# Kernel tuning notes

Hardware: AMD Instinct MI355X
Metric: run time of the kernel (lower is better)

Reference implementation:

```python
import jax, jax.numpy as jnp
import numpy as np

B, S, V, E, HID = 16, 40, 1004, 256, 256
C, R, HW = 1024, 256, 32  # featureChannel, releMapChannel, spatial
BN_EPS = 1e-5


def setup_inputs() -> dict:
    key = jax.random.key(0)
    ks = jax.random.split(key, 16)
    sc = 0.05
    emb = jax.random.normal(ks[4], (V, E), jnp.float32) * sc
    emb = emb.at[0].set(0.0)  # padding_idx = 0
    return {
        "feature": jax.random.normal(ks[0], (B, C, HW, HW), jnp.float32),
        "depth": jax.random.uniform(ks[1], (B, 1, HW, HW), jnp.float32),
        "instruction_idx": jax.random.randint(ks[2], (B, S), 0, V, jnp.int32),
        "instruction_length": jnp.clip(jax.random.randint(ks[3], (B,), 1, S + 1, jnp.int32), 1, S),
        "only_train_rele": 1,
        "emb_table": emb,
        "w_ih": jax.random.normal(ks[5], (4 * HID, E), jnp.float32) * sc,
        "w_hh": jax.random.normal(ks[6], (4 * HID, HID), jnp.float32) * sc,
        "b_ih": jax.random.normal(ks[7], (4 * HID,), jnp.float32) * sc,
        "b_hh": jax.random.normal(ks[8], (4 * HID,), jnp.float32) * sc,
        "e2d_w": jax.random.normal(ks[9], (HID, HID), jnp.float32) * sc,
        "e2d_b": jax.random.normal(ks[10], (HID,), jnp.float32) * sc,
        "lin1_w": jax.random.normal(ks[11], (R * C, HID), jnp.float32) * sc,
        "lin1_b": jax.random.normal(ks[12], (R * C,), jnp.float32) * sc,
        "bn_gamma": jnp.ones((R,), jnp.float32),
        "bn_beta": jnp.zeros((R,), jnp.float32),
        "bn_mean": jax.random.normal(ks[13], (R,), jnp.float32) * 0.01,
        "bn_var": jnp.ones((R,), jnp.float32),
    }


def _encoder_lstm(idx, lengths, emb_table, w_ih, w_hh, b_ih, b_hh, e2d_w, e2d_b):
    # Faithful to packed-sequence LSTM: state stops updating at each sample's length.
    embeds = emb_table[idx]                      # [B,S,E]
    xs = jnp.swapaxes(embeds, 0, 1)              # [S,B,E]
    mask = (jnp.arange(S)[:, None] < lengths[None, :])  # [S,B]
    h0 = jnp.zeros((B, HID), embeds.dtype)
    c0 = jnp.zeros((B, HID), embeds.dtype)

    def step(carry, xm):
        h, c = carry
        x_t, m = xm                              # [B,E], [B]
        gates = x_t @ w_ih.T + h @ w_hh.T + (b_ih + b_hh)  # [B,4H]
        i, f, g, o = jnp.split(gates, 4, axis=-1)  # torch gate order: i,f,g,o
        c_new = jax.nn.sigmoid(f) * c + jax.nn.sigmoid(i) * jnp.tanh(g)
        h_new = jax.nn.sigmoid(o) * jnp.tanh(c_new)
        m = m[:, None]
        return (jnp.where(m, h_new, h), jnp.where(m, c_new, c)), None

    (h_t, _), _ = jax.lax.scan(step, (h0, c0), (xs, mask))
    return jnp.tanh(h_t @ e2d_w.T + e2d_b)       # [B,HID]


def reference(feature, depth, instruction_idx, instruction_length, only_train_rele,
              emb_table, w_ih, w_hh, b_ih, b_hh, e2d_w, e2d_b,
              lin1_w, lin1_b, bn_gamma, bn_beta, bn_mean, bn_var):
    instr = _encoder_lstm(instruction_idx, instruction_length, emb_table,
                          w_ih, w_hh, b_ih, b_hh, e2d_w, e2d_b)  # [B,HID]
    # per-sample dynamic 1x1 filters (dropout in eval mode -> identity)
    f1 = jax.nn.leaky_relu(instr @ lin1_w.T + lin1_b, negative_slope=0.01)
    f1 = f1.reshape(B, R, C)
    # batched per-sample 1x1 conv: one einsum replaces the batch loop of F.conv2d
    rele = jax.nn.relu(jnp.einsum('bchw,brc->brhw', feature, f1))  # [B,R,H,W]
    # BatchNorm2d in eval mode with running stats
    scale = bn_gamma / jnp.sqrt(bn_var + BN_EPS)
    rele = rele * scale[None, :, None, None] + (bn_beta - bn_mean * scale)[None, :, None, None]
    single = jnp.max(rele, axis=1)               # channel-max pooling -> [B,H,W]
    return jnp.clip(single, 0.0, 1.0)
```

## Files before the change

kernel.cpp:

```cpp
#include <hip/hip_runtime.h>
#include <hip/hip_fp16.h>
#include <math.h>

#define NB 16
#define SQ 40
#define HIDN 256
#define CC 1024
#define NROW 262144

#define AGENT __HIP_MEMORY_SCOPE_AGENT

__device__ __forceinline__ float sigf(float x){ return 1.0f/(1.0f+__expf(-x)); }

typedef _Float16 h2v __attribute__((ext_vector_type(2)));
typedef _Float16 f16x8 __attribute__((ext_vector_type(8)));
typedef float    f32x4 __attribute__((ext_vector_type(4)));

__device__ __forceinline__ float fd2(unsigned w, unsigned h, float acc){
  h2v a = __builtin_bit_cast(h2v, w);
  h2v b = __builtin_bit_cast(h2v, h);
#if __has_builtin(__builtin_amdgcn_fdot2)
  return __builtin_amdgcn_fdot2(a, b, acc, false);
#else
  return acc + (float)a.x*(float)b.x + (float)a.y*(float)b.y;
#endif
}

__device__ __forceinline__ unsigned pkh(float lo, float hi){
  return (unsigned)__half_as_ushort(__float2half_rn(lo))
       | ((unsigned)__half_as_ushort(__float2half_rn(hi)) << 16);
}

__global__ __launch_bounds__(256) void k_xgates(
    const int* __restrict__ idx, const float* __restrict__ emb,
    const float* __restrict__ w_ih, const float* __restrict__ b_ih,
    const float* __restrict__ b_hh, float* __restrict__ XG)
{
  __shared__ float xs[8*256];
  int t = threadIdx.x;
  int tb0 = blockIdx.x * 8;
  #pragma unroll
  for (int i = 0; i < 8; ++i) {
    int flat = t + i*256;
    int p = flat >> 8, k = flat & 255;
    int tb = tb0 + p;
    int ts = tb >> 4, b = tb & 15;
    int row = idx[b*SQ + ts];
    xs[p*256 + k] = emb[row*256 + k];
  }
  __syncthreads();
  int rows[4];
  float acc[4][8];
  #pragma unroll
  for (int r = 0; r < 4; ++r) {
    rows[r] = t + r*256;
    float bias = b_ih[rows[r]] + b_hh[rows[r]];
    #pragma unroll
    for (int p = 0; p < 8; ++p) acc[r][p] = bias;
  }
  for (int k16 = 0; k16 < 16; ++k16) {
    float4 w[4][4];
    #pragma unroll
    for (int r = 0; r < 4; ++r)
      #pragma unroll
      for (int q = 0; q < 4; ++q)
        w[r][q] = *(const float4*)&w_ih[rows[r]*256 + k16*16 + q*4];
    #pragma unroll
    for (int p = 0; p < 8; ++p) {
      #pragma unroll
      for (int q = 0; q < 4; ++q) {
        float4 x = *(const float4*)&xs[p*256 + k16*16 + q*4];
        #pragma unroll
        for (int r = 0; r < 4; ++r)
          acc[r][p] += w[r][q].x*x.x + w[r][q].y*x.y + w[r][q].z*x.z + w[r][q].w*x.w;
      }
    }
  }
  #pragma unroll
  for (int p = 0; p < 8; ++p)
    #pragma unroll
    for (int r = 0; r < 4; ++r)
      XG[(tb0 + p)*1024 + rows[r]] = acc[r][p];
}

__global__ __launch_bounds__(256) void k_whh2(const float* __restrict__ w, uint4* __restrict__ W2)
{
  int tid = blockIdx.x*256 + threadIdx.x;
  int p   = tid >> 12;
  int oct = (tid >> 7) & 31;
  int r   = tid & 127;
  int gr  = (r >> 5)*256 + p*32 + (r & 31);
  const float* src = &w[gr*256 + oct*8];
  float4 a = *(const float4*)src;
  float4 b = *(const float4*)(src + 4);
  uint4 o;
  o.x = pkh(a.x, a.y);
  o.y = pkh(a.z, a.w);
  o.z = pkh(b.x, b.y);
  o.w = pkh(b.z, b.w);
  W2[tid] = o;
}

__global__ __launch_bounds__(256) void k_lstm_persist(
    const float* __restrict__ XG, const uint4* __restrict__ W2,
    const int* __restrict__ lens, const float* __restrict__ e2d_w,
    const float* __restrict__ e2d_b, float* __restrict__ instr,
    unsigned* __restrict__ hcomm, unsigned* __restrict__ flags)
{
  __shared__ uint4 wlds[32*128];
  __shared__ float dot_s[256];
  __shared__ float h_s[32];
  __shared__ float h_e[256];

  int t = threadIdx.x;
  int b = blockIdx.x >> 3;
  int p = blockIdx.x & 7;
  int len = lens[b];

  const uint4* Wp = W2 + p*4096;
  #pragma unroll
  for (int i = 0; i < 16; ++i) wlds[i*256 + t] = Wp[i*256 + t];
  __syncthreads();

  int r  = t & 127;
  int kh = t >> 7;
  int g  = r >> 5, u = r & 31;
  int xg_row = g*256 + p*32 + u;
  int lane = t & 63;

  unsigned* flag_b = flags + b*16;

  float c_reg = 0.0f, h_reg = 0.0f;

  for (int it = 0; it < SQ; ++it) {
    if (it > 0) {
      if (t == 0) {
        while (__hip_atomic_load(flag_b, __ATOMIC_ACQUIRE, AGENT) < (unsigned)(8*it))
          __builtin_amdgcn_s_sleep(2);
      }
      __syncthreads();
    }
    unsigned hp0 = 0u, hp1 = 0u;
    if (it > 0) {
      const unsigned long long* hc64 =
        (const unsigned long long*)(hcomm + (it & 1)*2048 + b*128);
      unsigned long long v = __hip_atomic_load(&hc64[lane], __ATOMIC_RELAXED, AGENT);
      hp0 = (unsigned)v; hp1 = (unsigned)(v >> 32);
    }
    int hp0i = (int)hp0, hp1i = (int)hp1;

    float a0, a1;
    if (kh == 0) { a0 = XG[(it*NB + b)*1024 + xg_row]; a1 = 0.0f; }
    else         { a0 = 0.0f;                           a1 = 0.0f; }

    int obase = kh*16;
    #pragma unroll
    for (int j = 0; j < 16; ++j) {
      int oct = obase + j;
      uint4 w4 = wlds[oct*128 + r];
      unsigned ha = (unsigned)__builtin_amdgcn_readlane(hp0i, 2*oct);
      unsigned hb = (unsigned)__builtin_amdgcn_readlane(hp1i, 2*oct);
      unsigned hc = (unsigned)__builtin_amdgcn_readlane(hp0i, 2*oct + 1);
      unsigned hd = (unsigned)__builtin_amdgcn_readlane(hp1i, 2*oct + 1);
      a0 = fd2(w4.x, ha, a0);
      a1 = fd2(w4.y, hb, a1);
      a0 = fd2(w4.z, hc, a0);
      a1 = fd2(w4.w, hd, a1);
    }
    dot_s[t] = a0 + a1;
    __syncthreads();

    if (t < 32) {
      float iv = sigf (dot_s[t]       + dot_s[t + 128]);
      float fv = sigf (dot_s[t + 32]  + dot_s[t + 160]);
      float gv = tanhf(dot_s[t + 64]  + dot_s[t + 192]);
      float ov = sigf (dot_s[t + 96]  + dot_s[t + 224]);
      float cn = fv*c_reg + iv*gv;
      float hn = ov*tanhf(cn);
      if (it < len) { c_reg = cn; h_reg = hn; }
      h_s[t] = h_reg;
    }
    __syncthreads();

    if (t < 16) {
      unsigned pk = pkh(h_s[2*t], h_s[2*t + 1]);
      __hip_atomic_store(&hcomm[((it + 1) & 1)*2048 + b*128 + p*16 + t], pk,
                         __ATOMIC_RELAXED, AGENT);
    }
    __syncthreads();
    if (t == 0)
      __hip_atomic_fetch_add(flag_b, 1u, __ATOMIC_RELEASE, AGENT);
  }

  if (p == 0) {
    if (t == 0) {
      while (__hip_atomic_load(flag_b, __ATOMIC_ACQUIRE, AGENT) < (unsigned)(8*SQ))
        __builtin_amdgcn_s_sleep(2);
    }
    __syncthreads();
    if (t < 64) {
      const unsigned long long* hc64 = (const unsigned long long*)(hcomm + 0*2048 + b*128);
      unsigned long long v = __hip_atomic_load(&hc64[t], __ATOMIC_RELAXED, AGENT);
      h2v lo = __builtin_bit_cast(h2v, (unsigned)v);
      h2v hi = __builtin_bit_cast(h2v, (unsigned)(v >> 32));
      h_e[4*t + 0] = (float)lo.x;
      h_e[4*t + 1] = (float)lo.y;
      h_e[4*t + 2] = (float)hi.x;
      h_e[4*t + 3] = (float)hi.y;
    }
    __syncthreads();
    float acc = e2d_b[t];
    const float4* wp = (const float4*)&e2d_w[t*256];
    #pragma unroll 8
    for (int k4 = 0; k4 < 64; ++k4) {
      float4 w = wp[k4];
      float4 h4 = *(const float4*)&h_e[k4*4];
      acc += w.x*h4.x + w.y*h4.y + w.z*h4.z + w.w*h4.w;
    }
    instr[b*256 + t] = tanhf(acc);
  }
}

__global__ __launch_bounds__(256) void k_lin1(
    const float* __restrict__ instr, const float* __restrict__ w,
    const float* __restrict__ bias, _Float16* __restrict__ f1h)
{
  __shared__ float is[4096];
  int t = threadIdx.x;
  #pragma unroll
  for (int i = 0; i < 16; ++i) is[t + i*256] = instr[t + i*256];
  __syncthreads();
  int r0 = blockIdx.x*512 + t;
  int r1 = r0 + 256;
  const float* w0 = &w[(size_t)r0*256];
  const float* w1 = &w[(size_t)r1*256];
  float acc0[16], acc1[16];
  float bz0 = bias[r0], bz1 = bias[r1];
  #pragma unroll
  for (int i = 0; i < 16; ++i){ acc0[i]=bz0; acc1[i]=bz1; }
  for (int k16 = 0; k16 < 16; ++k16) {
    float4 a[4], bb[4];
    #pragma unroll
    for (int q = 0; q < 4; ++q){
      a[q]  = *(const float4*)&w0[k16*16 + q*4];
      bb[q] = *(const float4*)&w1[k16*16 + q*4];
    }
    #pragma unroll
    for (int bi = 0; bi < 16; ++bi) {
      #pragma unroll
      for (int q = 0; q < 4; ++q) {
        float4 x = *(const float4*)&is[bi*256 + k16*16 + q*4];
        acc0[bi] += a[q].x*x.x + a[q].y*x.y + a[q].z*x.z + a[q].w*x.w;
        acc1[bi] += bb[q].x*x.x + bb[q].y*x.y + bb[q].z*x.z + bb[q].w*x.w;
      }
    }
  }
  #pragma unroll
  for (int bi = 0; bi < 16; ++bi) {
    float v0 = acc0[bi]; v0 = v0 > 0.0f ? v0 : 0.01f*v0;
    float v1 = acc1[bi]; v1 = v1 > 0.0f ? v1 : 0.01f*v1;
    f1h[(size_t)bi*NROW + r0] = (_Float16)v0;
    f1h[(size_t)bi*NROW + r1] = (_Float16)v1;
  }
}

__global__ __launch_bounds__(256, 1) void k_einsum_mfma(
    const uint4* __restrict__ f1h4, const float* __restrict__ feat,
    const float* __restrict__ gamma, const float* __restrict__ beta,
    const float* __restrict__ mean, const float* __restrict__ var,
    float* __restrict__ out)
{
  __shared__ unsigned ALDS[256*20];
  __shared__ unsigned BLDS[128*20];
  __shared__ float sc_s[256], sh_s[256];
  __shared__ float red[2][128];

  int t = threadIdx.x;
  int b  = blockIdx.x >> 3;
  int P0 = (blockIdx.x & 7) * 128;
  int wid  = t >> 6, lane = t & 63;
  int wp = wid & 1, wr = wid >> 1;
  int col = lane & 15, quad = lane >> 4;

  {
    float s = gamma[t] * rsqrtf(var[t] + 1e-5f);
    sc_s[t] = s;
    sh_s[t] = beta[t] - mean[t]*s;
  }

  f32x4 acc[8][4];
  #pragma unroll
  for (int mt = 0; mt < 8; ++mt)
    #pragma unroll
    for (int nt = 0; nt < 4; ++nt) acc[mt][nt] = (f32x4)0.0f;

  const uint4* arow = f1h4 + ((size_t)b*NROW + (size_t)t*1024)/8;
  int p_loc = t & 127, khalf = t >> 7;
  const float* bbase = feat + ((size_t)b*1024 + khalf*16)*1024 + P0 + p_loc;

  uint4 apf[4];
  float bpf[16];
  #pragma unroll
  for (int g = 0; g < 4; ++g) apf[g] = arow[g];
  #pragma unroll
  for (int j = 0; j < 16; ++j) bpf[j] = bbase[(size_t)j*1024];

  for (int kc = 0; kc < 32; ++kc) {
    __syncthreads();
    #pragma unroll
    for (int g = 0; g < 4; ++g)
      *(uint4*)&ALDS[t*20 + g*4] = apf[g];
    {
      unsigned u[8];
      #pragma unroll
      for (int i = 0; i < 8; ++i) u[i] = pkh(bpf[2*i], bpf[2*i+1]);
      uint4 w0 = {u[0],u[1],u[2],u[3]}, w1 = {u[4],u[5],u[6],u[7]};
      *(uint4*)&BLDS[p_loc*20 + khalf*8]     = w0;
      *(uint4*)&BLDS[p_loc*20 + khalf*8 + 4] = w1;
    }
    __syncthreads();
    if (kc + 1 < 32) {
      #pragma unroll
      for (int g = 0; g < 4; ++g) apf[g] = arow[(kc+1)*4 + g];
      const float* bb = bbase + (size_t)(kc+1)*32*1024;
      #pragma unroll
      for (int j = 0; j < 16; ++j) bpf[j] = bb[(size_t)j*1024];
    }
    f16x8 bf[4];
    #pragma unroll
    for (int nt = 0; nt < 4; ++nt) {
      uint4 raw = *(const uint4*)&BLDS[(wp*64 + nt*16 + col)*20 + quad*4];
      bf[nt] = __builtin_bit_cast(f16x8, raw);
    }
    #pragma unroll
    for (int mt = 0; mt < 8; ++mt) {
      uint4 raw = *(const uint4*)&ALDS[(wr*128 + mt*16 + col)*20 + quad*4];
      f16x8 af = __builtin_bit_cast(f16x8, raw);
      #pragma unroll
      for (int nt = 0; nt < 4; ++nt)
        acc[mt][nt] = __builtin_amdgcn_mfma_f32_16x16x32_f16(af, bf[nt], acc[mt][nt], 0, 0, 0);
    }
  }

  float pmax[4];
  #pragma unroll
  for (int nt = 0; nt < 4; ++nt) pmax[nt] = -3.4e38f;
  #pragma unroll
  for (int mt = 0; mt < 8; ++mt) {
    int rb = wr*128 + mt*16 + quad*4;
    f32x4 scv = *(const f32x4*)&sc_s[rb];
    f32x4 shv = *(const f32x4*)&sh_s[rb];
    #pragma unroll
    for (int nt = 0; nt < 4; ++nt) {
      f32x4 a = acc[mt][nt];
      #pragma unroll
      for (int reg = 0; reg < 4; ++reg) {
        float v = fmaxf(a[reg], 0.0f)*scv[reg] + shv[reg];
        pmax[nt] = fmaxf(pmax[nt], v);
      }
    }
  }
  #pragma unroll
  for (int nt = 0; nt < 4; ++nt) {
    float m = pmax[nt];
    m = fmaxf(m, __shfl_xor(m, 16));
    m = fmaxf(m, __shfl_xor(m, 32));
    if (lane < 16) red[wr][wp*64 + nt*16 + lane] = m;
  }
  __syncthreads();
  if (t < 128) {
    float v = fmaxf(red[0][t], red[1][t]);
    out[b*1024 + P0 + t] = fminf(fmaxf(v, 0.0f), 1.0f);
  }
}

extern "C" void kernel_launch(void* const* d_in, const int* in_sizes, int n_in,
                              void* d_out, int out_size, void* d_ws, size_t ws_size,
                              hipStream_t stream)
{
  const float* feature = (const float*)d_in[0];
  const int*   idx     = (const int*)d_in[2];
  const int*   lens    = (const int*)d_in[3];
  const float* emb     = (const float*)d_in[5];
  const float* w_ih    = (const float*)d_in[6];
  const float* w_hh    = (const float*)d_in[7];
  const float* b_ih    = (const float*)d_in[8];
  const float* b_hh    = (const float*)d_in[9];
  const float* e2d_w   = (const float*)d_in[10];
  const float* e2d_b   = (const float*)d_in[11];
  const float* lin1_w  = (const float*)d_in[12];
  const float* lin1_b  = (const float*)d_in[13];
  const float* gamma   = (const float*)d_in[14];
  const float* beta    = (const float*)d_in[15];
  const float* mean    = (const float*)d_in[16];
  const float* var     = (const float*)d_in[17];

  char* ws = (char*)d_ws;
  float*    XG     = (float*)(ws);
  float*    instr  = (float*)(ws + 2621440);
  uint4*    W2     = (uint4*)(ws + 2637824);
  unsigned* hcomm  = (unsigned*)(ws + 3162112);
  unsigned* flags  = (unsigned*)(ws + 3178496);
  _Float16* f1h    = (_Float16*)(ws + 3179520);

  hipMemsetAsync(flags, 0, 1024, stream);
  k_xgates      <<<80,  256, 0, stream>>>(idx, emb, w_ih, b_ih, b_hh, XG);
  k_whh2        <<<128, 256, 0, stream>>>(w_hh, W2);
  k_lstm_persist<<<128, 256, 0, stream>>>(XG, W2, lens, e2d_w, e2d_b, instr, hcomm, flags);
  k_lin1        <<<512, 256, 0, stream>>>(instr, lin1_w, lin1_b, f1h);
  k_einsum_mfma <<<128, 256, 0, stream>>>((const uint4*)f1h, feature, gamma, beta, mean, var,
                                          (float*)d_out);
}
```

Measured before the change: 697.3 us.

## Split LSTM recurrence across two register-resident blocks per sample with sentinel-based exchange

Replaces the 8-blocks-per-sample persistent LSTM, which used a shared atomic counter barrier, with 2 blocks of 512 threads per sample. Each block keeps its half of W_hh as fp16 in registers (128 dwords per thread). Hidden-state halves are exchanged through a per-timestep slot buffer that is pre-filled with a sentinel value, so consumers can poll for data directly instead of waiting on flag barriers. Each block computes the dot product with its own half of h before it waits for the other half, which overlaps local work with cross-block communication. The cost is high register pressure, a larger memset, and correctness that depends on no packed fp16 h pair ever equalling the sentinel bit pattern.

```diff
diff --git a/kernel.cpp b/kernel.cpp
--- a/kernel.cpp
+++ b/kernel.cpp
@@ -9,6 +9,7 @@
 #define NROW 262144
 
 #define AGENT __HIP_MEMORY_SCOPE_AGENT
+#define SENT 0x7E7E7E7Eu
 
 __device__ __forceinline__ float sigf(float x){ return 1.0f/(1.0f+__expf(-x)); }
 
@@ -83,141 +84,123 @@
       XG[(tb0 + p)*1024 + rows[r]] = acc[r][p];
 }
 
-__global__ __launch_bounds__(256) void k_whh2(const float* __restrict__ w, uint4* __restrict__ W2)
+__global__ __launch_bounds__(256) void k_whh3(const float* __restrict__ w, unsigned* __restrict__ W3)
 {
   int tid = blockIdx.x*256 + threadIdx.x;
-  int p   = tid >> 12;
-  int oct = (tid >> 7) & 31;
-  int r   = tid & 127;
-  int gr  = (r >> 5)*256 + p*32 + (r & 31);
-  const float* src = &w[gr*256 + oct*8];
-  float4 a = *(const float4*)src;
-  float4 b = *(const float4*)(src + 4);
-  uint4 o;
-  o.x = pkh(a.x, a.y);
-  o.y = pkh(a.z, a.w);
-  o.z = pkh(b.x, b.y);
-  o.w = pkh(b.z, b.w);
-  W2[tid] = o;
-}
-
-__global__ __launch_bounds__(256) void k_lstm_persist(
-    const float* __restrict__ XG, const uint4* __restrict__ W2,
+  int c    = tid & 3;
+  int tt   = (tid >> 2) & 511;
+  int q    = (tid >> 11) & 31;
+  int half = tid >> 16;
+  int pair = 4*q + c;
+  int g = tt >> 7, j = tt & 127;
+  int row = g*256 + half*128 + j;
+  float2 v = *(const float2*)&w[(size_t)row*256 + 2*pair];
+  W3[tid] = pkh(v.x, v.y);
+}
+
+__global__ __launch_bounds__(512) void k_lstm2(
+    const float* __restrict__ XG, const uint4* __restrict__ W3,
     const int* __restrict__ lens, const float* __restrict__ e2d_w,
     const float* __restrict__ e2d_b, float* __restrict__ instr,
-    unsigned* __restrict__ hcomm, unsigned* __restrict__ flags)
-{
-  __shared__ uint4 wlds[32*128];
-  __shared__ float dot_s[256];
-  __shared__ float h_s[32];
+    unsigned* __restrict__ hcomm)
+{
+  __shared__ float dot_s[512];
+  __shared__ float h_s[128];
   __shared__ float h_e[256];
 
   int t = threadIdx.x;
-  int b = blockIdx.x >> 3;
-  int p = blockIdx.x & 7;
-  int len = lens[b];
-
-  const uint4* Wp = W2 + p*4096;
-  #pragma unroll
-  for (int i = 0; i < 16; ++i) wlds[i*256 + t] = Wp[i*256 + t];
-  __syncthreads();
-
-  int r  = t & 127;
-  int kh = t >> 7;
-  int g  = r >> 5, u = r & 31;
-  int xg_row = g*256 + p*32 + u;
+  int b    = blockIdx.x & 15;
+  int half = blockIdx.x >> 4;
+  int len  = lens[b];
   int lane = t & 63;
 
-  unsigned* flag_b = flags + b*16;
-
+  unsigned wv[128];
+  {
+    const uint4* wp = W3 + (size_t)half*32*512 + t;
+    #pragma unroll
+    for (int q = 0; q < 32; ++q) {
+      uint4 v = wp[(size_t)q*512];
+      wv[4*q+0]=v.x; wv[4*q+1]=v.y; wv[4*q+2]=v.z; wv[4*q+3]=v.w;
+    }
+  }
+
+  int g = t >> 7, j = t & 127;
+  int row = g*256 + half*128 + j;
   float c_reg = 0.0f, h_reg = 0.0f;
 
   for (int it = 0; it < SQ; ++it) {
+    float acc = XG[(it*NB + b)*1024 + row];
     if (it > 0) {
-      if (t == 0) {
-        while (__hip_atomic_load(flag_b, __ATOMIC_ACQUIRE, AGENT) < (unsigned)(8*it))
-          __builtin_amdgcn_s_sleep(2);
-      }
-      __syncthreads();
-    }
-    unsigned hp0 = 0u, hp1 = 0u;
-    if (it > 0) {
-      const unsigned long long* hc64 =
-        (const unsigned long long*)(hcomm + (it & 1)*2048 + b*128);
-      unsigned long long v = __hip_atomic_load(&hc64[lane], __ATOMIC_RELAXED, AGENT);
-      hp0 = (unsigned)v; hp1 = (unsigned)(v >> 32);
-    }
-    int hp0i = (int)hp0, hp1i = (int)hp1;
-
-    float a0, a1;
-    if (kh == 0) { a0 = XG[(it*NB + b)*1024 + xg_row]; a1 = 0.0f; }
-    else         { a0 = 0.0f;                           a1 = 0.0f; }
-
-    int obase = kh*16;
-    #pragma unroll
-    for (int j = 0; j < 16; ++j) {
-      int oct = obase + j;
-      uint4 w4 = wlds[oct*128 + r];
-      unsigned ha = (unsigned)__builtin_amdgcn_readlane(hp0i, 2*oct);
-      unsigned hb = (unsigned)__builtin_amdgcn_readlane(hp1i, 2*oct);
-      unsigned hc = (unsigned)__builtin_amdgcn_readlane(hp0i, 2*oct + 1);
-      unsigned hd = (unsigned)__builtin_amdgcn_readlane(hp1i, 2*oct + 1);
-      a0 = fd2(w4.x, ha, a0);
-      a1 = fd2(w4.y, hb, a1);
-      a0 = fd2(w4.z, hc, a0);
-      a1 = fd2(w4.w, hd, a1);
-    }
-    dot_s[t] = a0 + a1;
-    __syncthreads();
-
-    if (t < 32) {
-      float iv = sigf (dot_s[t]       + dot_s[t + 128]);
-      float fv = sigf (dot_s[t + 32]  + dot_s[t + 160]);
-      float gv = tanhf(dot_s[t + 64]  + dot_s[t + 192]);
-      float ov = sigf (dot_s[t + 96]  + dot_s[t + 224]);
+      unsigned own = pkh(h_s[2*lane], h_s[2*lane + 1]);
+      int owni = (int)own;
+      const unsigned* oslot = hcomm + ((it-1)*NB + b)*128 + (half ? 0 : 64);
+      if (half == 0) {
+        #pragma unroll
+        for (int q = 0; q < 64; ++q)
+          acc = fd2(wv[q], (unsigned)__builtin_amdgcn_readlane(owni, q), acc);
+        unsigned oth;
+        do { oth = __hip_atomic_load(oslot + lane, __ATOMIC_RELAXED, AGENT); }
+        while (__any((int)(oth == SENT)));
+        int othi = (int)oth;
+        #pragma unroll
+        for (int q = 0; q < 64; ++q)
+          acc = fd2(wv[64+q], (unsigned)__builtin_amdgcn_readlane(othi, q), acc);
+      } else {
+        #pragma unroll
+        for (int q = 0; q < 64; ++q)
+          acc = fd2(wv[64+q], (unsigned)__builtin_amdgcn_readlane(owni, q), acc);
+        unsigned oth;
+        do { oth = __hip_atomic_load(oslot + lane, __ATOMIC_RELAXED, AGENT); }
+        while (__any((int)(oth == SENT)));
+        int othi = (int)oth;
+        #pragma unroll
+        for (int q = 0; q < 64; ++q)
+          acc = fd2(wv[q], (unsigned)__builtin_amdgcn_readlane(othi, q), acc);
+      }
+    }
+    dot_s[t] = acc;
+    __syncthreads();
+    if (t < 128) {
+      float iv = sigf (dot_s[t]);
+      float fv = sigf (dot_s[t + 128]);
+      float gv = tanhf(dot_s[t + 256]);
+      float ov = sigf (dot_s[t + 384]);
       float cn = fv*c_reg + iv*gv;
       float hn = ov*tanhf(cn);
       if (it < len) { c_reg = cn; h_reg = hn; }
       h_s[t] = h_reg;
     }
     __syncthreads();
-
-    if (t < 16) {
-      unsigned pk = pkh(h_s[2*t], h_s[2*t + 1]);
-      __hip_atomic_store(&hcomm[((it + 1) & 1)*2048 + b*128 + p*16 + t], pk,
-                         __ATOMIC_RELAXED, AGENT);
-    }
-    __syncthreads();
-    if (t == 0)
-      __hip_atomic_fetch_add(flag_b, 1u, __ATOMIC_RELEASE, AGENT);
-  }
-
-  if (p == 0) {
-    if (t == 0) {
-      while (__hip_atomic_load(flag_b, __ATOMIC_ACQUIRE, AGENT) < (unsigned)(8*SQ))
-        __builtin_amdgcn_s_sleep(2);
-    }
-    __syncthreads();
+    if (t < 64)
+      __hip_atomic_store(hcomm + (it*NB + b)*128 + half*64 + t,
+                         pkh(h_s[2*t], h_s[2*t+1]), __ATOMIC_RELAXED, AGENT);
+  }
+
+  if (half == 0) {
+    const unsigned* slot = hcomm + ((SQ-1)*NB + b)*128;
     if (t < 64) {
-      const unsigned long long* hc64 = (const unsigned long long*)(hcomm + 0*2048 + b*128);
-      unsigned long long v = __hip_atomic_load(&hc64[t], __ATOMIC_RELAXED, AGENT);
-      h2v lo = __builtin_bit_cast(h2v, (unsigned)v);
-      h2v hi = __builtin_bit_cast(h2v, (unsigned)(v >> 32));
-      h_e[4*t + 0] = (float)lo.x;
-      h_e[4*t + 1] = (float)lo.y;
-      h_e[4*t + 2] = (float)hi.x;
-      h_e[4*t + 3] = (float)hi.y;
-    }
-    __syncthreads();
-    float acc = e2d_b[t];
-    const float4* wp = (const float4*)&e2d_w[t*256];
-    #pragma unroll 8
-    for (int k4 = 0; k4 < 64; ++k4) {
-      float4 w = wp[k4];
-      float4 h4 = *(const float4*)&h_e[k4*4];
-      acc += w.x*h4.x + w.y*h4.y + w.z*h4.z + w.w*h4.w;
-    }
-    instr[b*256 + t] = tanhf(acc);
+      unsigned v0, v1;
+      do {
+        v0 = __hip_atomic_load(slot + t,      __ATOMIC_RELAXED, AGENT);
+        v1 = __hip_atomic_load(slot + 64 + t, __ATOMIC_RELAXED, AGENT);
+      } while (__any((int)(v0 == SENT)) || __any((int)(v1 == SENT)));
+      h2v lo = __builtin_bit_cast(h2v, v0);
+      h2v hi = __builtin_bit_cast(h2v, v1);
+      h_e[2*t]       = (float)lo.x;  h_e[2*t + 1]       = (float)lo.y;
+      h_e[128 + 2*t] = (float)hi.x;  h_e[128 + 2*t + 1] = (float)hi.y;
+    }
+    __syncthreads();
+    if (t < 256) {
+      float acc2 = e2d_b[t];
+      const float4* wp2 = (const float4*)&e2d_w[t*256];
+      #pragma unroll 8
+      for (int k4 = 0; k4 < 64; ++k4) {
+        float4 w = wp2[k4];
+        float4 h4 = *(const float4*)&h_e[k4*4];
+        acc2 += w.x*h4.x + w.y*h4.y + w.z*h4.z + w.w*h4.w;
+      }
+      instr[b*256 + t] = tanhf(acc2);
+    }
   }
 }
 
@@ -398,16 +381,15 @@
   char* ws = (char*)d_ws;
   float*    XG     = (float*)(ws);
   float*    instr  = (float*)(ws + 2621440);
-  uint4*    W2     = (uint4*)(ws + 2637824);
+  unsigned* W3     = (unsigned*)(ws + 2637824);
   unsigned* hcomm  = (unsigned*)(ws + 3162112);
-  unsigned* flags  = (unsigned*)(ws + 3178496);
-  _Float16* f1h    = (_Float16*)(ws + 3179520);
-
-  hipMemsetAsync(flags, 0, 1024, stream);
-  k_xgates      <<<80,  256, 0, stream>>>(idx, emb, w_ih, b_ih, b_hh, XG);
-  k_whh2        <<<128, 256, 0, stream>>>(w_hh, W2);
-  k_lstm_persist<<<128, 256, 0, stream>>>(XG, W2, lens, e2d_w, e2d_b, instr, hcomm, flags);
-  k_lin1        <<<512, 256, 0, stream>>>(instr, lin1_w, lin1_b, f1h);
+  _Float16* f1h    = (_Float16*)(ws + 3489792);
+
+  hipMemsetAsync(hcomm, 0x7E, 327680, stream);
+  k_xgates <<<80,  256, 0, stream>>>(idx, emb, w_ih, b_ih, b_hh, XG);
+  k_whh3   <<<512, 256, 0, stream>>>(w_hh, W3);
+  k_lstm2  <<<32,  512, 0, stream>>>(XG, (const uint4*)W3, lens, e2d_w, e2d_b, instr, hcomm);
+  k_lin1   <<<512, 256, 0, stream>>>(instr, lin1_w, lin1_b, f1h);
   k_einsum_mfma <<<128, 256, 0, stream>>>((const uint4*)f1h, feature, gamma, beta, mean, var,
                                           (float*)d_out);
 }
```

Result: faster. 614.7 us (-11.8%).
